# Kernel optimization log

Measured on AMD Instinct MI355X. Metric: run time of the kernel, lower is better.

Reference implementation:

```python
import jax, jax.numpy as jnp
import numpy as np

B, T, H, W, C = 2, 8, 64, 64, 192
WIN = (4, 8, 8)
SHIFT = (2, 4, 4)
HEADS = 6
HID = 4 * C
N = WIN[0] * WIN[1] * WIN[2]  # 256 tokens per window
CPB_HID = 512


def window_partition(x, win):
    b, t, h, w, c = x.shape
    x = x.reshape(b, t // win[0], win[0], h // win[1], win[1], w // win[2], win[2], c)
    x = x.transpose(0, 1, 3, 5, 2, 4, 6, 7)
    return x.reshape(-1, win[0] * win[1] * win[2], c)


def window_reverse(wins, win, b, t, h, w):
    x = wins.reshape(b, t // win[0], h // win[1], w // win[2], win[0], win[1], win[2], -1)
    x = x.transpose(0, 1, 4, 2, 5, 3, 6, 7)
    return x.reshape(b, t, h, w, -1)


def _rel_coords_table():
    axes = [np.arange(-(WIN[i] - 1), WIN[i], dtype=np.float32) for i in range(3)]
    tbl = np.stack(np.meshgrid(*axes, indexing='ij'), axis=-1)  # (2wt-1,2wh-1,2ww-1,3)
    for i in range(3):
        tbl[..., i] /= WIN[i] - 1
    tbl *= 8.0
    tbl = np.sign(tbl) * np.log2(np.abs(tbl) + 1.0) / np.log2(8.0)
    return tbl.reshape(-1, 3)


def _rel_pos_index():
    coords = np.stack(np.meshgrid(np.arange(WIN[0]), np.arange(WIN[1]), np.arange(WIN[2]), indexing='ij'))
    cf = coords.reshape(3, -1)
    rel = (cf[:, :, None] - cf[:, None, :]).transpose(1, 2, 0)
    rel[..., 0] += WIN[0] - 1
    rel[..., 1] += WIN[1] - 1
    rel[..., 2] += WIN[2] - 1
    rel[..., 0] *= (2 * WIN[1] - 1) * (2 * WIN[2] - 1)
    rel[..., 1] *= 2 * WIN[2] - 1
    return rel.sum(-1)  # (N, N) int


def _attn_mask():
    img = np.zeros((1, T, H, W, 1), dtype=np.float32)
    cnt = 0
    for d in (slice(-WIN[0]), slice(-WIN[0], -SHIFT[0]), slice(-SHIFT[0], None)):
        for h in (slice(-WIN[1]), slice(-WIN[1], -SHIFT[1]), slice(-SHIFT[1], None)):
            for w in (slice(-WIN[2]), slice(-WIN[2], -SHIFT[2]), slice(-SHIFT[2], None)):
                img[:, d, h, w, :] = cnt
                cnt += 1
    mw = window_partition(img, WIN).squeeze(-1)  # (nW, N)
    am = mw[:, None, :] - mw[:, :, None]
    return np.where(am != 0, -100.0, 0.0).astype(np.float32)


REL_TABLE = jnp.asarray(_rel_coords_table())      # (M, 3)
RPI = jnp.asarray(_rel_pos_index().reshape(-1))   # (N*N,)
MASK = jnp.asarray(_attn_mask())                  # (nW, N, N)


def _ln(x, g, b):
    m = x.mean(-1, keepdims=True)
    v = x.var(-1, keepdims=True)
    return (x - m) / jnp.sqrt(v + 1e-5) * g + b


def setup_inputs() -> dict:
    key = jax.random.key(0)
    ks = jax.random.split(key, 16)
    s = lambda fan: 1.0 / np.sqrt(fan)
    return {
        'x': jax.random.normal(ks[0], (B, T, H, W, C), jnp.float32),
        'qkv_w': jax.random.normal(ks[1], (3 * C, C), jnp.float32) * s(C),
        'qkv_b': jnp.zeros((3 * C,), jnp.float32),
        'proj_w': jax.random.normal(ks[2], (C, C), jnp.float32) * s(C),
        'proj_b': jnp.zeros((C,), jnp.float32),
        'cpb_w1': jax.random.normal(ks[3], (CPB_HID, 3), jnp.float32) * s(3),
        'cpb_b1': jnp.zeros((CPB_HID,), jnp.float32),
        'cpb_w2': jax.random.normal(ks[4], (HEADS, CPB_HID), jnp.float32) * s(CPB_HID),
        'logit_scale': jnp.log(10.0 * jnp.ones((HEADS, 1, 1), jnp.float32)),
        'norm1_g': jnp.ones((C,), jnp.float32),
        'norm1_b': jnp.zeros((C,), jnp.float32),
        'norm2_g': jnp.ones((C,), jnp.float32),
        'norm2_b': jnp.zeros((C,), jnp.float32),
        'fc1_w': jax.random.normal(ks[5], (HID, C), jnp.float32) * s(C),
        'fc1_b': jnp.zeros((HID,), jnp.float32),
        'fc2_w': jax.random.normal(ks[6], (C, HID), jnp.float32) * s(HID),
        'fc2_b': jnp.zeros((C,), jnp.float32),
    }


def reference(x, qkv_w, qkv_b, proj_w, proj_b, cpb_w1, cpb_b1, cpb_w2,
              logit_scale, norm1_g, norm1_b, norm2_g, norm2_b,
              fc1_w, fc1_b, fc2_w, fc2_b):
    shortcut = x
    # cyclic shift
    xs = jnp.roll(x, shift=(-SHIFT[0], -SHIFT[1], -SHIFT[2]), axis=(1, 2, 3))
    xw = window_partition(xs, WIN)  # (B*nW, N, C)
    B_ = xw.shape[0]
    d = C // HEADS
    qkv = (xw @ qkv_w.T + qkv_b).reshape(B_, N, 3, HEADS, d).transpose(2, 0, 3, 1, 4)
    q, k, v = qkv[0], qkv[1], qkv[2]  # (B_, h, N, d)
    # cosine attention (F.normalize eps=1e-12)
    qn = q / jnp.maximum(jnp.linalg.norm(q, axis=-1, keepdims=True), 1e-12)
    kn = k / jnp.maximum(jnp.linalg.norm(k, axis=-1, keepdims=True), 1e-12)
    attn = jnp.einsum('bhnd,bhmd->bhnm', qn, kn)
    scale = jnp.exp(jnp.minimum(logit_scale, jnp.log(100.0)))  # clamp at log(1/0.01)
    attn = attn * scale
    # continuous relative position bias
    tbl = jax.nn.relu(REL_TABLE @ cpb_w1.T + cpb_b1) @ cpb_w2.T  # (M, heads)
    bias = tbl[RPI].reshape(N, N, HEADS).transpose(2, 0, 1)      # (h, N, N)
    attn = attn + 16.0 * jax.nn.sigmoid(bias)[None]
    # shift mask
    nW = MASK.shape[0]
    attn = attn.reshape(B_ // nW, nW, HEADS, N, N) + MASK[None, :, None]
    attn = jax.nn.softmax(attn.reshape(B_, HEADS, N, N), axis=-1)
    out = jnp.einsum('bhnm,bhmd->bhnd', attn, v)
    out = out.transpose(0, 2, 1, 3).reshape(B_, N, C)
    out = out @ proj_w.T + proj_b
    xr = window_reverse(out, WIN, B, T, H, W)
    xr = jnp.roll(xr, shift=SHIFT, axis=(1, 2, 3))
    # SwinV2 res-post-norm residual
    x = shortcut + _ln(xr, norm1_g, norm1_b)
    h1 = jax.nn.gelu(x @ fc1_w.T + fc1_b, approximate=False)
    x = x + _ln(h1 @ fc2_w.T + fc2_b, norm2_g, norm2_b)
    return x
```

## Files before the change

kernel.cpp:

```cpp
#include <hip/hip_runtime.h>
#include <math.h>


typedef short short8 __attribute__((ext_vector_type(8)));
typedef short short4v __attribute__((ext_vector_type(4)));
typedef float f32x4 __attribute__((ext_vector_type(4)));

__device__ __forceinline__ short f2bf(float f) {
    union { float f; unsigned u; } v; v.f = f;
    unsigned r = v.u + 0x7FFF + ((v.u >> 16) & 1);
    return (short)(r >> 16);
}

__device__ __forceinline__ float gelu_fast(float x) {
    float s = x * x;
    float t = fmaf(0.044715f, s, 1.0f);
    float y = -1.5957691216057308f * x * t;
    return x / (1.0f + __expf(y));
}

__global__ __launch_bounds__(64) void pack_w_k(const float* __restrict__ w,
                                               short* __restrict__ dst, int K) {
    int lane = threadIdx.x;
    int ktn = K >> 5;
    int nt = blockIdx.x / ktn, kt = blockIdx.x % ktn;
    int r = lane & 15, q = lane >> 4;
    const float* src = w + (size_t)(nt * 16 + r) * K + kt * 32 + q * 8;
    short8 v;
#pragma unroll
    for (int j = 0; j < 8; j++) v[j] = f2bf(src[j]);
    ((short8*)dst)[(size_t)blockIdx.x * 64 + lane] = v;
}

__global__ __launch_bounds__(64) void cpb_table_k(const float* __restrict__ w1,
                                                  const float* __restrict__ b1,
                                                  const float* __restrict__ w2,
                                                  float* __restrict__ tbl6) {
    int m = blockIdx.x;
    int lane = threadIdx.x;
    int it = m / 225;
    int ih = (m / 15) % 15;
    int iw = m % 15;
    float r0 = (float)(it - 3) * (8.0f / 3.0f);
    float r1 = (float)(ih - 7) * (8.0f / 7.0f);
    float r2 = (float)(iw - 7) * (8.0f / 7.0f);
    float c0 = (r0 < 0.f ? -1.f : 1.f) * log2f(fabsf(r0) + 1.0f) * (1.0f / 3.0f);
    float c1 = (r1 < 0.f ? -1.f : 1.f) * log2f(fabsf(r1) + 1.0f) * (1.0f / 3.0f);
    float c2 = (r2 < 0.f ? -1.f : 1.f) * log2f(fabsf(r2) + 1.0f) * (1.0f / 3.0f);
    float hv[8];
#pragma unroll
    for (int j = 0; j < 8; j++) {
        int t = lane * 8 + j;
        hv[j] = fmaxf(0.0f, c0 * w1[3 * t] + c1 * w1[3 * t + 1] + c2 * w1[3 * t + 2] + b1[t]);
    }
#pragma unroll
    for (int head = 0; head < 6; head++) {
        float s = 0.f;
#pragma unroll
        for (int j = 0; j < 8; j++) s += hv[j] * w2[head * 512 + lane * 8 + j];
        s += __shfl_xor(s, 1);
        s += __shfl_xor(s, 2);
        s += __shfl_xor(s, 4);
        s += __shfl_xor(s, 8);
        s += __shfl_xor(s, 16);
        s += __shfl_xor(s, 32);
        if (lane == 0) tbl6[m * 6 + head] = s;
    }
}

__global__ __launch_bounds__(256) void bias_k(const float* __restrict__ tbl6,
                                              float* __restrict__ biasT) {
    int idx = blockIdx.x * 256 + threadIdx.x;
    int h = idx >> 16;
    int rem = idx & 65535;
    int jj = rem >> 8, ii = rem & 255;
    int dt = (ii >> 6) - (jj >> 6) + 3;
    int dh = ((ii >> 3) & 7) - ((jj >> 3) & 7) + 7;
    int dw = (ii & 7) - (jj & 7) + 7;
    int rel = dt * 225 + dh * 15 + dw;
    float v = tbl6[rel * 6 + h];
    biasT[idx] = 16.0f / (1.0f + expf(-v));
}

#define ZSTR 388
__global__ __launch_bounds__(256) void qkv_mfma_k(const float* __restrict__ x,
                                                  const short* __restrict__ wqp,
                                                  const float* __restrict__ qkv_b,
                                                  short* __restrict__ qbf,
                                                  short* __restrict__ kbf,
                                                  short* __restrict__ vtb) {
    __shared__ float Z[32 * ZSTR];
    int tid = threadIdx.x, lane = tid & 63, w = tid >> 6;
    int r = lane & 15, q = lane >> 4;
    int b_ = blockIdx.x >> 3, n0 = (blockIdx.x & 7) << 5;
    int b = b_ >> 7, win = b_ & 127;
    int wt = win >> 6, wh = (win >> 3) & 7, ww = win & 7;

    short8 af[2][6];
#pragma unroll
    for (int m = 0; m < 2; m++) {
        int n = n0 + m * 16 + r;
        int t0 = ((wt * 4 + (n >> 6)) + 2) & 7;
        int h0 = ((wh * 8 + ((n >> 3) & 7)) + 4) & 63;
        int w0 = ((ww * 8 + (n & 7)) + 4) & 63;
        const float* src = x + ((size_t)((b * 8 + t0) * 64 + h0) * 64 + w0) * 192 + q * 8;
#pragma unroll
        for (int kt = 0; kt < 6; kt++) {
            float4 x0 = *(const float4*)(src + kt * 32);
            float4 x1 = *(const float4*)(src + kt * 32 + 4);
            short8 v;
            v[0] = f2bf(x0.x); v[1] = f2bf(x0.y); v[2] = f2bf(x0.z); v[3] = f2bf(x0.w);
            v[4] = f2bf(x1.x); v[5] = f2bf(x1.y); v[6] = f2bf(x1.z); v[7] = f2bf(x1.w);
            af[m][kt] = v;
        }
    }

    for (int ntl = 0; ntl < 9; ntl++) {
        int nt = w * 9 + ntl;
        float bias = qkv_b[nt * 16 + r];
        short8 bfr[6];
#pragma unroll
        for (int kt = 0; kt < 6; kt++)
            bfr[kt] = ((const short8*)wqp)[(size_t)(nt * 6 + kt) * 64 + lane];
        f32x4 a0 = {bias, bias, bias, bias};
        f32x4 a1 = {bias, bias, bias, bias};
#pragma unroll
        for (int kt = 0; kt < 6; kt++) {
            a0 = __builtin_amdgcn_mfma_f32_16x16x32_bf16(af[0][kt], bfr[kt], a0, 0, 0, 0);
            a1 = __builtin_amdgcn_mfma_f32_16x16x32_bf16(af[1][kt], bfr[kt], a1, 0, 0, 0);
        }
        int col = nt * 16 + r;
        if (nt < 24) {
#pragma unroll
            for (int reg = 0; reg < 4; reg++) {
                Z[(q * 4 + reg) * ZSTR + col] = a0[reg];
                Z[(16 + q * 4 + reg) * ZSTR + col] = a1[reg];
            }
        } else {
            int ch = col - 384;
            int hh = ch >> 5, dd = ch & 31;
            short* vb = vtb + ((size_t)(b_ * 6 + hh) * 32 + dd) * 256 + n0;
            short4v p0, p1;
#pragma unroll
            for (int reg = 0; reg < 4; reg++) { p0[reg] = f2bf(a0[reg]); p1[reg] = f2bf(a1[reg]); }
            *(short4v*)(vb + q * 4) = p0;
            *(short4v*)(vb + 16 + q * 4) = p1;
        }
    }
    __syncthreads();
    for (int rw = tid; rw < 384; rw += 256) {
        int token = rw / 12, rr = rw - token * 12;
        int isq = rr < 6 ? 1 : 0;
        int h = isq ? rr : rr - 6;
        const float* rp = &Z[token * ZSTR + rr * 32];
        float ss = 0.f;
#pragma unroll
        for (int d = 0; d < 32; d++) ss += rp[d] * rp[d];
        float inv = 1.0f / fmaxf(sqrtf(ss), 1e-12f);
        short* dst = (isq ? qbf : kbf) + ((size_t)(b_ * 6 + h) * 256 + n0 + token) * 32;
#pragma unroll
        for (int d8 = 0; d8 < 4; d8++) {
            short8 v;
#pragma unroll
            for (int j = 0; j < 8; j++) v[j] = f2bf(rp[d8 * 8 + j] * inv);
            *(short8*)(dst + d8 * 8) = v;
        }
    }
}

#define KSTR 40
#define VSTR 264
#define PSTR 40
__global__ __launch_bounds__(256) void attn_mfma_k(const short* __restrict__ qbf,
                                                   const short* __restrict__ kbf,
                                                   const short* __restrict__ vtb,
                                                   const float* __restrict__ biasT,
                                                   const float* __restrict__ logit_scale,
                                                   float* __restrict__ att) {
    __shared__ short Ks[256 * KSTR];
    __shared__ short Vs[32 * VSTR];
    __shared__ short Ps[4][16 * PSTR];
    int tid = threadIdx.x, lane = tid & 63, w = tid >> 6;
    int r = lane & 15, q = lane >> 4;
    int b_ = blockIdx.x / 6, h = blockIdx.x % 6;
    size_t base = (size_t)(b_ * 6 + h) * 8192;

    const short8* kg = (const short8*)(kbf + base);
    const short8* vg = (const short8*)(vtb + base);
    for (int i = tid; i < 1024; i += 256) {
        short8 kv = kg[i];
        *(short8*)&Ks[(i >> 2) * KSTR + (i & 3) * 8] = kv;
        short8 vv = vg[i];
        *(short8*)&Vs[(i >> 5) * VSTR + (i & 31) * 8] = vv;
    }

    short8 qf[4];
#pragma unroll
    for (int mt = 0; mt < 4; mt++)
        qf[mt] = *(const short8*)(qbf + base + (size_t)(w * 64 + mt * 16 + r) * 32 + q * 8);

    float scale = __expf(fminf(logit_scale[h], 4.6051702f));
    float M = scale + 16.0f;
    int win = b_ & 127;
    int wt4 = (win >> 6) * 4, wh8 = ((win >> 3) & 7) * 8, ww8 = (win & 7) * 8;
    auto region = [&](int n) {
        int ts = wt4 + (n >> 6), hs = wh8 + ((n >> 3) & 7), wsv = ww8 + (n & 7);
        int rt = ts < 4 ? 0 : (ts < 6 ? 1 : 2);
        int rh = hs < 56 ? 0 : (hs < 60 ? 1 : 2);
        int rw = wsv < 56 ? 0 : (wsv < 60 ? 1 : 2);
        return rt * 9 + rh * 3 + rw;
    };
    int rowreg[4][4];
#pragma unroll
    for (int mt = 0; mt < 4; mt++)
#pragma unroll
        for (int reg = 0; reg < 4; reg++)
            rowreg[mt][reg] = region(w * 64 + mt * 16 + q * 4 + reg);

    f32x4 O[4][2];
    float lp[4][4];
#pragma unroll
    for (int mt = 0; mt < 4; mt++) {
        O[mt][0] = (f32x4){0.f, 0.f, 0.f, 0.f};
        O[mt][1] = (f32x4){0.f, 0.f, 0.f, 0.f};
#pragma unroll
        for (int reg = 0; reg < 4; reg++) lp[mt][reg] = 0.f;
    }
    __syncthreads();

    const float* bh = biasT + ((size_t)h << 16);
    for (int s = 0; s < 8; s++) {
        short8 kf0 = *(const short8*)&Ks[(s * 32 + r) * KSTR + q * 8];
        short8 kf1 = *(const short8*)&Ks[(s * 32 + 16 + r) * KSTR + q * 8];
        short8 vf0 = *(const short8*)&Vs[r * VSTR + s * 32 + q * 8];
        short8 vf1 = *(const short8*)&Vs[(16 + r) * VSTR + s * 32 + q * 8];
        int cr0 = region(s * 32 + r);
        int cr1 = region(s * 32 + 16 + r);
#pragma unroll
        for (int mt = 0; mt < 4; mt++) {
            f32x4 s0 = {0.f, 0.f, 0.f, 0.f};
            f32x4 s1 = {0.f, 0.f, 0.f, 0.f};
            s0 = __builtin_amdgcn_mfma_f32_16x16x32_bf16(qf[mt], kf0, s0, 0, 0, 0);
            s1 = __builtin_amdgcn_mfma_f32_16x16x32_bf16(qf[mt], kf1, s1, 0, 0, 0);
            int qcol = w * 64 + mt * 16 + q * 4;
            float4 b0 = *(const float4*)(bh + (size_t)(s * 32 + r) * 256 + qcol);
            float4 b1 = *(const float4*)(bh + (size_t)(s * 32 + 16 + r) * 256 + qcol);
#pragma unroll
            for (int reg = 0; reg < 4; reg++) {
                float bb0 = (reg == 0 ? b0.x : reg == 1 ? b0.y : reg == 2 ? b0.z : b0.w);
                float bb1 = (reg == 0 ? b1.x : reg == 1 ? b1.y : reg == 2 ? b1.z : b1.w);
                float v0 = s0[reg] * scale + bb0 + (cr0 == rowreg[mt][reg] ? 0.f : -100.f) - M;
                float v1 = s1[reg] * scale + bb1 + (cr1 == rowreg[mt][reg] ? 0.f : -100.f) - M;
                float p0 = __expf(v0);
                float p1 = __expf(v1);
                lp[mt][reg] += p0 + p1;
                Ps[w][(q * 4 + reg) * PSTR + r] = f2bf(p0);
                Ps[w][(q * 4 + reg) * PSTR + 16 + r] = f2bf(p1);
            }
            short8 pa = *(const short8*)&Ps[w][r * PSTR + q * 8];
            O[mt][0] = __builtin_amdgcn_mfma_f32_16x16x32_bf16(pa, vf0, O[mt][0], 0, 0, 0);
            O[mt][1] = __builtin_amdgcn_mfma_f32_16x16x32_bf16(pa, vf1, O[mt][1], 0, 0, 0);
        }
    }

#pragma unroll
    for (int mt = 0; mt < 4; mt++)
#pragma unroll
        for (int reg = 0; reg < 4; reg++) {
            float v = lp[mt][reg];
            v += __shfl_xor(v, 1);
            v += __shfl_xor(v, 2);
            v += __shfl_xor(v, 4);
            v += __shfl_xor(v, 8);
            lp[mt][reg] = 1.0f / v;
        }
#pragma unroll
    for (int mt = 0; mt < 4; mt++)
#pragma unroll
        for (int nt = 0; nt < 2; nt++)
#pragma unroll
            for (int reg = 0; reg < 4; reg++) {
                int query = w * 64 + mt * 16 + q * 4 + reg;
                att[((size_t)b_ * 256 + query) * 192 + h * 32 + nt * 16 + r] =
                    O[mt][nt][reg] * lp[mt][reg];
            }
}

__global__ __launch_bounds__(256) void proj_mfma_k(const float* __restrict__ att,
                                                   const short* __restrict__ wpp,
                                                   const float* __restrict__ proj_b,
                                                   const float* __restrict__ x,
                                                   const float* __restrict__ g1,
                                                   const float* __restrict__ b1n,
                                                   float* __restrict__ out,
                                                   short* __restrict__ xmb) {
    __shared__ float Z[32 * 196];
    __shared__ float ps[32][8];
    __shared__ float pss[32][8];
    __shared__ float mean_s[32], inv_s[32];
    int tid = threadIdx.x, lane = tid & 63, w = tid >> 6;
    int r = lane & 15, q = lane >> 4;
    int b_ = blockIdx.x >> 3, n0 = (blockIdx.x & 7) << 5;

    short8 af[2][6];
#pragma unroll
    for (int m = 0; m < 2; m++) {
        const float* src = att + ((size_t)b_ * 256 + n0 + m * 16 + r) * 192 + q * 8;
#pragma unroll
        for (int kt = 0; kt < 6; kt++) {
            float4 x0 = *(const float4*)(src + kt * 32);
            float4 x1 = *(const float4*)(src + kt * 32 + 4);
            short8 v;
            v[0] = f2bf(x0.x); v[1] = f2bf(x0.y); v[2] = f2bf(x0.z); v[3] = f2bf(x0.w);
            v[4] = f2bf(x1.x); v[5] = f2bf(x1.y); v[6] = f2bf(x1.z); v[7] = f2bf(x1.w);
            af[m][kt] = v;
        }
    }
    for (int ntl = 0; ntl < 3; ntl++) {
        int nt = w * 3 + ntl;
        f32x4 binit = *(const f32x4*)(proj_b + nt * 16 + q * 4);
        short8 bfr[6];
#pragma unroll
        for (int kt = 0; kt < 6; kt++)
            bfr[kt] = ((const short8*)wpp)[(size_t)(nt * 6 + kt) * 64 + lane];
        f32x4 a0 = binit, a1 = binit;
#pragma unroll
        for (int kt = 0; kt < 6; kt++) {
            a0 = __builtin_amdgcn_mfma_f32_16x16x32_bf16(bfr[kt], af[0][kt], a0, 0, 0, 0);
            a1 = __builtin_amdgcn_mfma_f32_16x16x32_bf16(bfr[kt], af[1][kt], a1, 0, 0, 0);
        }
        *(f32x4*)&Z[(r) * 196 + nt * 16 + q * 4] = a0;
        *(f32x4*)&Z[(16 + r) * 196 + nt * 16 + q * 4] = a1;
    }
    __syncthreads();
    {
        int token = tid >> 3, part = tid & 7;
        float s = 0.f, ss = 0.f;
        const float* zr = &Z[token * 196 + part * 24];
#pragma unroll
        for (int c = 0; c < 24; c++) { float v = zr[c]; s += v; ss += v * v; }
        ps[token][part] = s; pss[token][part] = ss;
    }
    __syncthreads();
    if (tid < 32) {
        float s = 0.f, ss = 0.f;
#pragma unroll
        for (int p = 0; p < 8; p++) { s += ps[tid][p]; ss += pss[tid][p]; }
        float mean = s * (1.0f / 192.0f);
        float var = ss * (1.0f / 192.0f) - mean * mean;
        mean_s[tid] = mean;
        inv_s[tid] = 1.0f / sqrtf(var + 1e-5f);
    }
    __syncthreads();
    int b = b_ >> 7, win = b_ & 127;
    int wt = win >> 6, wh = (win >> 3) & 7, ww = win & 7;
    for (int idx = tid; idx < 6144; idx += 256) {
        int token = idx / 192;
        int ch = idx - token * 192;
        int n = n0 + token;
        int t0 = ((wt * 4 + (n >> 6)) + 2) & 7;
        int h0 = ((wh * 8 + ((n >> 3) & 7)) + 4) & 63;
        int w0 = ((ww * 8 + (n & 7)) + 4) & 63;
        size_t gb = ((size_t)((b * 8 + t0) * 64 + h0) * 64 + w0) * 192;
        float v = (Z[token * 196 + ch] - mean_s[token]) * inv_s[token] * g1[ch] + b1n[ch];
        float o = x[gb + ch] + v;
        out[gb + ch] = o;
        xmb[gb + ch] = f2bf(o);
    }
}

#define HSTR 776
__global__ __launch_bounds__(512, 4) void mlp_mfma_k(const short* __restrict__ xmb,
                                                     const short* __restrict__ w1p,
                                                     const short* __restrict__ w2p,
                                                     const float* __restrict__ fc1_b,
                                                     const float* __restrict__ fc2_b,
                                                     const float* __restrict__ g2,
                                                     const float* __restrict__ b2,
                                                     float* __restrict__ out) {
    __shared__ short Hs[32 * HSTR];
    __shared__ float ps[32][16];
    __shared__ float pss[32][16];
    __shared__ float mean_s[32], inv_s[32];
    int tid = threadIdx.x;
    int lane = tid & 63, w = tid >> 6;
    int r = lane & 15, q = lane >> 4;
    size_t tok0 = (size_t)blockIdx.x * 32;

    short8 af[2][6];
#pragma unroll
    for (int m = 0; m < 2; m++)
#pragma unroll
        for (int kt = 0; kt < 6; kt++)
            af[m][kt] = *(const short8*)(xmb + (tok0 + m * 16 + r) * 192 + kt * 32 + q * 8);

    {
        short8 bw[2][6];
        int nt0 = w * 6;
#pragma unroll
        for (int kt = 0; kt < 6; kt++)
            bw[0][kt] = ((const short8*)w1p)[(size_t)(nt0 * 6 + kt) * 64 + lane];
        for (int ntl = 0; ntl < 6; ntl++) {
            int nt = nt0 + ntl;
            int cur = ntl & 1, nxt = cur ^ 1;
            int ntn = (ntl < 5) ? nt + 1 : nt;
#pragma unroll
            for (int kt = 0; kt < 6; kt++)
                bw[nxt][kt] = ((const short8*)w1p)[(size_t)(ntn * 6 + kt) * 64 + lane];
            f32x4 binit = *(const f32x4*)(fc1_b + nt * 16 + q * 4);
            f32x4 acc0 = binit, acc1 = binit;
#pragma unroll
            for (int kt = 0; kt < 6; kt++) {
                acc0 = __builtin_amdgcn_mfma_f32_16x16x32_bf16(bw[cur][kt], af[0][kt], acc0, 0, 0, 0);
                acc1 = __builtin_amdgcn_mfma_f32_16x16x32_bf16(bw[cur][kt], af[1][kt], acc1, 0, 0, 0);
            }
            short4v p0, p1;
#pragma unroll
            for (int reg = 0; reg < 4; reg++) {
                p0[reg] = f2bf(gelu_fast(acc0[reg]));
                p1[reg] = f2bf(gelu_fast(acc1[reg]));
            }
            *(short4v*)&Hs[(r) * HSTR + nt * 16 + q * 4] = p0;
            *(short4v*)&Hs[(16 + r) * HSTR + nt * 16 + q * 4] = p1;
        }
    }
    __syncthreads();

    int odd = w & 1;
    int ntA = (3 * w) >> 1, ntB = ntA + 1;
    f32x4 acc2[3];
#pragma unroll
    for (int i = 0; i < 3; i++) acc2[i] = (f32x4){0.f, 0.f, 0.f, 0.f};
    {
        short8 bA = ((const short8*)w2p)[(size_t)(ntA * 24 + 0) * 64 + lane];
        short8 bB = ((const short8*)w2p)[(size_t)(ntB * 24 + 0) * 64 + lane];
        for (int kk = 0; kk < 24; kk++) {
            int kn = (kk < 23) ? kk + 1 : kk;
            short8 bAn = ((const short8*)w2p)[(size_t)(ntA * 24 + kn) * 64 + lane];
            short8 bBn = ((const short8*)w2p)[(size_t)(ntB * 24 + kn) * 64 + lane];
            short8 a0 = *(const short8*)&Hs[r * HSTR + kk * 32 + q * 8];
            short8 a1 = *(const short8*)&Hs[(16 + r) * HSTR + kk * 32 + q * 8];
            if (!odd) {
                acc2[0] = __builtin_amdgcn_mfma_f32_16x16x32_bf16(bA, a0, acc2[0], 0, 0, 0);
                acc2[1] = __builtin_amdgcn_mfma_f32_16x16x32_bf16(bA, a1, acc2[1], 0, 0, 0);
                acc2[2] = __builtin_amdgcn_mfma_f32_16x16x32_bf16(bB, a0, acc2[2], 0, 0, 0);
            } else {
                acc2[0] = __builtin_amdgcn_mfma_f32_16x16x32_bf16(bA, a1, acc2[0], 0, 0, 0);
                acc2[1] = __builtin_amdgcn_mfma_f32_16x16x32_bf16(bB, a0, acc2[1], 0, 0, 0);
                acc2[2] = __builtin_amdgcn_mfma_f32_16x16x32_bf16(bB, a1, acc2[2], 0, 0, 0);
            }
            bA = bAn; bB = bBn;
        }
    }
    __syncthreads();
    float* Z = (float*)Hs;
    {
        int tnts[3], tms[3];
        tnts[0] = ntA; tms[0] = odd;
        tnts[1] = odd ? ntB : ntA; tms[1] = odd ? 0 : 1;
        tnts[2] = ntB; tms[2] = odd;
#pragma unroll
        for (int i = 0; i < 3; i++) {
            f32x4 b4 = *(const f32x4*)(fc2_b + tnts[i] * 16 + q * 4);
            f32x4 zv = acc2[i] + b4;
            *(f32x4*)&Z[(tms[i] * 16 + r) * 196 + tnts[i] * 16 + q * 4] = zv;
        }
    }
    __syncthreads();

    {
        int token = tid >> 4, part = tid & 15;
        float s = 0.f, ss = 0.f;
        const float* zr = &Z[token * 196 + part * 12];
#pragma unroll
        for (int c = 0; c < 12; c++) { float v = zr[c]; s += v; ss += v * v; }
        ps[token][part] = s; pss[token][part] = ss;
    }
    __syncthreads();
    if (tid < 32) {
        float s = 0.f, ss = 0.f;
#pragma unroll
        for (int p = 0; p < 16; p++) { s += ps[tid][p]; ss += pss[tid][p]; }
        float mean = s * (1.0f / 192.0f);
        float var = ss * (1.0f / 192.0f) - mean * mean;
        mean_s[tid] = mean;
        inv_s[tid] = 1.0f / sqrtf(var + 1e-5f);
    }
    __syncthreads();
    for (int rep = 0; rep < 12; rep++) {
        int idx = rep * 512 + tid;
        int token = idx / 192;
        int ch = idx - token * 192;
        float v = (Z[token * 196 + ch] - mean_s[token]) * inv_s[token] * g2[ch] + b2[ch];
        size_t gi = (tok0 + token) * 192 + ch;
        out[gi] = out[gi] + v;
    }
}

extern "C" void kernel_launch(void* const* d_in, const int* in_sizes, int n_in,
                              void* d_out, int out_size, void* d_ws, size_t ws_size,
                              hipStream_t stream) {
    const float* x           = (const float*)d_in[0];
    const float* qkv_w       = (const float*)d_in[1];
    const float* qkv_b       = (const float*)d_in[2];
    const float* proj_w      = (const float*)d_in[3];
    const float* proj_b      = (const float*)d_in[4];
    const float* cpb_w1      = (const float*)d_in[5];
    const float* cpb_b1      = (const float*)d_in[6];
    const float* cpb_w2      = (const float*)d_in[7];
    const float* logit_scale = (const float*)d_in[8];
    const float* norm1_g     = (const float*)d_in[9];
    const float* norm1_b     = (const float*)d_in[10];
    const float* norm2_g     = (const float*)d_in[11];
    const float* norm2_b     = (const float*)d_in[12];
    const float* fc1_w       = (const float*)d_in[13];
    const float* fc1_b       = (const float*)d_in[14];
    const float* fc2_w       = (const float*)d_in[15];
    const float* fc2_b       = (const float*)d_in[16];
    float* out = (float*)d_out;

    float* ws = (float*)d_ws;
    const size_t QKVE = (size_t)256 * 6 * 256 * 32;
    float* att    = ws;
    float* biasT  = att + QKVE;
    float* tbl6   = biasT + (size_t)6 * 256 * 256;
    short* w1pack = (short*)(tbl6 + 9472);
    short* w2pack = w1pack + (size_t)768 * 192;
    short* wqpack = w2pack + (size_t)192 * 768;
    short* wppack = wqpack + (size_t)576 * 192;
    short* qbf    = wppack + (size_t)192 * 192;
    short* kbf    = qbf + QKVE;
    short* vtb    = kbf + QKVE;
    short* xmb    = vtb + QKVE;

    hipLaunchKernelGGL(pack_w_k, dim3(288), dim3(64), 0, stream, fc1_w, w1pack, 192);
    hipLaunchKernelGGL(pack_w_k, dim3(288), dim3(64), 0, stream, fc2_w, w2pack, 768);
    hipLaunchKernelGGL(pack_w_k, dim3(216), dim3(64), 0, stream, qkv_w, wqpack, 192);
    hipLaunchKernelGGL(pack_w_k, dim3(72), dim3(64), 0, stream, proj_w, wppack, 192);
    hipLaunchKernelGGL(cpb_table_k, dim3(1575), dim3(64), 0, stream, cpb_w1, cpb_b1, cpb_w2, tbl6);
    hipLaunchKernelGGL(bias_k, dim3(1536), dim3(256), 0, stream, tbl6, biasT);
    hipLaunchKernelGGL(qkv_mfma_k, dim3(2048), dim3(256), 0, stream, x, wqpack, qkv_b, qbf, kbf, vtb);
    hipLaunchKernelGGL(attn_mfma_k, dim3(1536), dim3(256), 0, stream, qbf, kbf, vtb, biasT, logit_scale, att);
    hipLaunchKernelGGL(proj_mfma_k, dim3(2048), dim3(256), 0, stream, att, wppack, proj_b, x, norm1_g, norm1_b, out, xmb);
    hipLaunchKernelGGL(mlp_mfma_k, dim3(2048), dim3(512), 0, stream, xmb, w1pack, w2pack,
                       fc1_b, fc2_b, norm2_g, norm2_b, out);
}
```

Baseline: 422.8 us.

## Restructure MLP kernel to 64-token tiles with chunked hidden dimension

The MLP kernel now processes 64 tokens per block instead of 32, staging the input tile in shared memory. The 768-wide hidden layer is computed in three 256-column chunks, each consumed right away by the fc2 accumulation, which keeps the hidden buffer small. Each weight fragment is reused across twice as many tokens, roughly halving weight traffic per token. The LayerNorm reduction uses wave shuffles instead of a two-stage shared-memory reduction. In exchange there are more barriers per block, more accumulator registers, and half as many blocks.

```diff
diff --git a/kernel.cpp b/kernel.cpp
--- a/kernel.cpp
+++ b/kernel.cpp
@@ -369,7 +369,9 @@
     }
 }
 
-#define HSTR 776
+#define XSTR 200
+#define H2STR 264
+#define ZFSTR 196
 __global__ __launch_bounds__(512, 4) void mlp_mfma_k(const short* __restrict__ xmb,
                                                      const short* __restrict__ w1p,
                                                      const short* __restrict__ w2p,
@@ -378,120 +380,118 @@
                                                      const float* __restrict__ g2,
                                                      const float* __restrict__ b2,
                                                      float* __restrict__ out) {
-    __shared__ short Hs[32 * HSTR];
-    __shared__ float ps[32][16];
-    __shared__ float pss[32][16];
-    __shared__ float mean_s[32], inv_s[32];
+    __shared__ short Buf[64 * XSTR + 64 * H2STR];
+    short* Xs = Buf;
+    short* Hs = Buf + 64 * XSTR;
+    float* Z = (float*)Buf;
+    __shared__ float mean_s[64], inv_s[64];
     int tid = threadIdx.x;
     int lane = tid & 63, w = tid >> 6;
     int r = lane & 15, q = lane >> 4;
-    size_t tok0 = (size_t)blockIdx.x * 32;
-
-    short8 af[2][6];
-#pragma unroll
-    for (int m = 0; m < 2; m++)
-#pragma unroll
-        for (int kt = 0; kt < 6; kt++)
-            af[m][kt] = *(const short8*)(xmb + (tok0 + m * 16 + r) * 192 + kt * 32 + q * 8);
+    size_t tok0 = (size_t)blockIdx.x * 64;
+
+    for (int i = tid; i < 1536; i += 512) {
+        int token = i / 24, ch8 = (i - token * 24) * 8;
+        short8 v = *(const short8*)(xmb + (tok0 + token) * 192 + ch8);
+        *(short8*)&Xs[token * XSTR + ch8] = v;
+    }
+    __syncthreads();
+
+    int mg = w >> 2;
+    int ng = w & 3;
+    f32x4 acc2[6];
+#pragma unroll
+    for (int i = 0; i < 6; i++) acc2[i] = (f32x4){0.f, 0.f, 0.f, 0.f};
+
+    for (int c = 0; c < 3; c++) {
+        {
+            int ntg0 = c * 16 + 2 * w;
+            f32x4 a[2][4];
+#pragma unroll
+            for (int ntl = 0; ntl < 2; ntl++) {
+                f32x4 binit = *(const f32x4*)(fc1_b + (ntg0 + ntl) * 16 + q * 4);
+#pragma unroll
+                for (int m = 0; m < 4; m++) a[ntl][m] = binit;
+            }
+#pragma unroll
+            for (int kt = 0; kt < 6; kt++) {
+                short8 w0 = ((const short8*)w1p)[(size_t)((ntg0) * 6 + kt) * 64 + lane];
+                short8 w1f = ((const short8*)w1p)[(size_t)((ntg0 + 1) * 6 + kt) * 64 + lane];
+                short8 xb[4];
+#pragma unroll
+                for (int m = 0; m < 4; m++)
+                    xb[m] = *(const short8*)&Xs[(m * 16 + r) * XSTR + kt * 32 + q * 8];
+#pragma unroll
+                for (int m = 0; m < 4; m++) {
+                    a[0][m] = __builtin_amdgcn_mfma_f32_16x16x32_bf16(w0, xb[m], a[0][m], 0, 0, 0);
+                    a[1][m] = __builtin_amdgcn_mfma_f32_16x16x32_bf16(w1f, xb[m], a[1][m], 0, 0, 0);
+                }
+            }
+#pragma unroll
+            for (int ntl = 0; ntl < 2; ntl++) {
+                int hcol = (2 * w + ntl) * 16 + q * 4;
+#pragma unroll
+                for (int m = 0; m < 4; m++) {
+                    short4v p;
+#pragma unroll
+                    for (int reg = 0; reg < 4; reg++) p[reg] = f2bf(gelu_fast(a[ntl][m][reg]));
+                    *(short4v*)&Hs[(m * 16 + r) * H2STR + hcol] = p;
+                }
+            }
+        }
+        __syncthreads();
+
+#pragma unroll
+        for (int kk = 0; kk < 8; kk++) {
+            short8 hb0 = *(const short8*)&Hs[((mg * 2) * 16 + r) * H2STR + kk * 32 + q * 8];
+            short8 hb1 = *(const short8*)&Hs[((mg * 2 + 1) * 16 + r) * H2STR + kk * 32 + q * 8];
+            int kkg = c * 8 + kk;
+#pragma unroll
+            for (int n = 0; n < 3; n++) {
+                int ntz = ng * 3 + n;
+                short8 wf = ((const short8*)w2p)[(size_t)(ntz * 24 + kkg) * 64 + lane];
+                acc2[n * 2 + 0] = __builtin_amdgcn_mfma_f32_16x16x32_bf16(wf, hb0, acc2[n * 2 + 0], 0, 0, 0);
+                acc2[n * 2 + 1] = __builtin_amdgcn_mfma_f32_16x16x32_bf16(wf, hb1, acc2[n * 2 + 1], 0, 0, 0);
+            }
+        }
+        __syncthreads();
+    }
+
+#pragma unroll
+    for (int n = 0; n < 3; n++) {
+        int ntz = ng * 3 + n;
+        f32x4 b4 = *(const f32x4*)(fc2_b + ntz * 16 + q * 4);
+#pragma unroll
+        for (int mh = 0; mh < 2; mh++) {
+            int token = (mg * 2 + mh) * 16 + r;
+            f32x4 zv = acc2[n * 2 + mh] + b4;
+            *(f32x4*)&Z[token * ZFSTR + ntz * 16 + q * 4] = zv;
+        }
+    }
+    __syncthreads();
 
     {
-        short8 bw[2][6];
-        int nt0 = w * 6;
-#pragma unroll
-        for (int kt = 0; kt < 6; kt++)
-            bw[0][kt] = ((const short8*)w1p)[(size_t)(nt0 * 6 + kt) * 64 + lane];
-        for (int ntl = 0; ntl < 6; ntl++) {
-            int nt = nt0 + ntl;
-            int cur = ntl & 1, nxt = cur ^ 1;
-            int ntn = (ntl < 5) ? nt + 1 : nt;
-#pragma unroll
-            for (int kt = 0; kt < 6; kt++)
-                bw[nxt][kt] = ((const short8*)w1p)[(size_t)(ntn * 6 + kt) * 64 + lane];
-            f32x4 binit = *(const f32x4*)(fc1_b + nt * 16 + q * 4);
-            f32x4 acc0 = binit, acc1 = binit;
-#pragma unroll
-            for (int kt = 0; kt < 6; kt++) {
-                acc0 = __builtin_amdgcn_mfma_f32_16x16x32_bf16(bw[cur][kt], af[0][kt], acc0, 0, 0, 0);
-                acc1 = __builtin_amdgcn_mfma_f32_16x16x32_bf16(bw[cur][kt], af[1][kt], acc1, 0, 0, 0);
-            }
-            short4v p0, p1;
-#pragma unroll
-            for (int reg = 0; reg < 4; reg++) {
-                p0[reg] = f2bf(gelu_fast(acc0[reg]));
-                p1[reg] = f2bf(gelu_fast(acc1[reg]));
-            }
-            *(short4v*)&Hs[(r) * HSTR + nt * 16 + q * 4] = p0;
-            *(short4v*)&Hs[(16 + r) * HSTR + nt * 16 + q * 4] = p1;
-        }
-    }
-    __syncthreads();
-
-    int odd = w & 1;
-    int ntA = (3 * w) >> 1, ntB = ntA + 1;
-    f32x4 acc2[3];
-#pragma unroll
-    for (int i = 0; i < 3; i++) acc2[i] = (f32x4){0.f, 0.f, 0.f, 0.f};
-    {
-        short8 bA = ((const short8*)w2p)[(size_t)(ntA * 24 + 0) * 64 + lane];
-        short8 bB = ((const short8*)w2p)[(size_t)(ntB * 24 + 0) * 64 + lane];
-        for (int kk = 0; kk < 24; kk++) {
-            int kn = (kk < 23) ? kk + 1 : kk;
-            short8 bAn = ((const short8*)w2p)[(size_t)(ntA * 24 + kn) * 64 + lane];
-            short8 bBn = ((const short8*)w2p)[(size_t)(ntB * 24 + kn) * 64 + lane];
-            short8 a0 = *(const short8*)&Hs[r * HSTR + kk * 32 + q * 8];
-            short8 a1 = *(const short8*)&Hs[(16 + r) * HSTR + kk * 32 + q * 8];
-            if (!odd) {
-                acc2[0] = __builtin_amdgcn_mfma_f32_16x16x32_bf16(bA, a0, acc2[0], 0, 0, 0);
-                acc2[1] = __builtin_amdgcn_mfma_f32_16x16x32_bf16(bA, a1, acc2[1], 0, 0, 0);
-                acc2[2] = __builtin_amdgcn_mfma_f32_16x16x32_bf16(bB, a0, acc2[2], 0, 0, 0);
-            } else {
-                acc2[0] = __builtin_amdgcn_mfma_f32_16x16x32_bf16(bA, a1, acc2[0], 0, 0, 0);
-                acc2[1] = __builtin_amdgcn_mfma_f32_16x16x32_bf16(bB, a0, acc2[1], 0, 0, 0);
-                acc2[2] = __builtin_amdgcn_mfma_f32_16x16x32_bf16(bB, a1, acc2[2], 0, 0, 0);
-            }
-            bA = bAn; bB = bBn;
-        }
-    }
-    __syncthreads();
-    float* Z = (float*)Hs;
-    {
-        int tnts[3], tms[3];
-        tnts[0] = ntA; tms[0] = odd;
-        tnts[1] = odd ? ntB : ntA; tms[1] = odd ? 0 : 1;
-        tnts[2] = ntB; tms[2] = odd;
-#pragma unroll
-        for (int i = 0; i < 3; i++) {
-            f32x4 b4 = *(const f32x4*)(fc2_b + tnts[i] * 16 + q * 4);
-            f32x4 zv = acc2[i] + b4;
-            *(f32x4*)&Z[(tms[i] * 16 + r) * 196 + tnts[i] * 16 + q * 4] = zv;
-        }
-    }
-    __syncthreads();
-
-    {
-        int token = tid >> 4, part = tid & 15;
+        int token = w * 8 + (lane >> 3), part = lane & 7;
         float s = 0.f, ss = 0.f;
-        const float* zr = &Z[token * 196 + part * 12];
-#pragma unroll
-        for (int c = 0; c < 12; c++) { float v = zr[c]; s += v; ss += v * v; }
-        ps[token][part] = s; pss[token][part] = ss;
-    }
-    __syncthreads();
-    if (tid < 32) {
-        float s = 0.f, ss = 0.f;
-#pragma unroll
-        for (int p = 0; p < 16; p++) { s += ps[tid][p]; ss += pss[tid][p]; }
-        float mean = s * (1.0f / 192.0f);
-        float var = ss * (1.0f / 192.0f) - mean * mean;
-        mean_s[tid] = mean;
-        inv_s[tid] = 1.0f / sqrtf(var + 1e-5f);
-    }
-    __syncthreads();
-    for (int rep = 0; rep < 12; rep++) {
+        const float* zr = &Z[token * ZFSTR + part * 24];
+#pragma unroll
+        for (int ccc = 0; ccc < 24; ccc++) { float v = zr[ccc]; s += v; ss += v * v; }
+        s += __shfl_xor(s, 1); ss += __shfl_xor(ss, 1);
+        s += __shfl_xor(s, 2); ss += __shfl_xor(ss, 2);
+        s += __shfl_xor(s, 4); ss += __shfl_xor(ss, 4);
+        if (part == 0) {
+            float mean = s * (1.0f / 192.0f);
+            float var = ss * (1.0f / 192.0f) - mean * mean;
+            mean_s[token] = mean;
+            inv_s[token] = 1.0f / sqrtf(var + 1e-5f);
+        }
+    }
+    __syncthreads();
+    for (int rep = 0; rep < 24; rep++) {
         int idx = rep * 512 + tid;
         int token = idx / 192;
         int ch = idx - token * 192;
-        float v = (Z[token * 196 + ch] - mean_s[token]) * inv_s[token] * g2[ch] + b2[ch];
+        float v = (Z[token * ZFSTR + ch] - mean_s[token]) * inv_s[token] * g2[ch] + b2[ch];
         size_t gi = (tok0 + token) * 192 + ch;
         out[gi] = out[gi] + v;
     }
@@ -542,6 +542,6 @@
     hipLaunchKernelGGL(qkv_mfma_k, dim3(2048), dim3(256), 0, stream, x, wqpack, qkv_b, qbf, kbf, vtb);
     hipLaunchKernelGGL(attn_mfma_k, dim3(1536), dim3(256), 0, stream, qbf, kbf, vtb, biasT, logit_scale, att);
     hipLaunchKernelGGL(proj_mfma_k, dim3(2048), dim3(256), 0, stream, att, wppack, proj_b, x, norm1_g, norm1_b, out, xmb);
-    hipLaunchKernelGGL(mlp_mfma_k, dim3(2048), dim3(512), 0, stream, xmb, w1pack, w2pack,
+    hipLaunchKernelGGL(mlp_mfma_k, dim3(1024), dim3(512), 0, stream, xmb, w1pack, w2pack,
                        fc1_b, fc2_b, norm2_g, norm2_b, out);
 }
```

Result: no change. 419.3 us (-0.8%).
